# Kernel optimization log

Hardware: AMD Instinct MI355X
Metric: run time of the kernel (lower is better)

Reference implementation:

```python
import jax, jax.numpy as jnp
import numpy as np

B, P, Q, A, H = 8, 512, 64, 16, 128
H2, H10, G = 2 * H, 10 * H, 3 * H


def setup_inputs() -> dict:
    key = jax.random.key(0)
    ks = jax.random.split(key, 40)
    n = lambda k, s, sc=1.0: jax.random.normal(k, s, jnp.float32) * sc
    W = 0.05  # xavier-ish small init so tanh stays in linear-ish range
    inp = {
        "passage_enc": n(ks[0], (B, P, H2)),
        "query_enc": n(ks[1], (B, Q, H2)),
        "alt1_enc": n(ks[2], (B, A, H)),
        "alt2_enc": n(ks[3], (B, A, H)),
        "alt3_enc": n(ks[4], (B, A, H)),
        "a_att_w": n(ks[5], (H,), W),
        "Wc1": n(ks[6], (H2, H), W), "Wc2": n(ks[7], (H2, H), W), "vc": n(ks[8], (H,), W),
        "Wb": n(ks[9], (H2, H2), W),
        "Wd": n(ks[10], (H2, H), W), "vd": n(ks[11], (H,), W),
        "Wm": n(ks[12], (H2, H), W), "vm": n(ks[13], (H,), W),
        "wq": n(ks[14], (H2, H), W), "vq": n(ks[15], (H,), W),
        "wp1": n(ks[16], (H2, H), W), "wp2": n(ks[17], (H2, H), W), "vp": n(ks[18], (H,), W),
        "predict_w": n(ks[19], (H2, H), W),
        "gWih_f": n(ks[20], (H10, G), W), "gWhh_f": n(ks[21], (H, G), W),
        "gbih_f": jnp.zeros((G,), jnp.float32), "gbhh_f": jnp.zeros((G,), jnp.float32),
        "gWih_b": n(ks[22], (H10, G), W), "gWhh_b": n(ks[23], (H, G), W),
        "gbih_b": jnp.zeros((G,), jnp.float32), "gbhh_b": jnp.zeros((G,), jnp.float32),
        "passage_mask": jnp.ones((B, P), jnp.int32),
        "query_mask": jnp.ones((B, Q), jnp.int32),
        "alt1_mask": jnp.ones((B, A), jnp.int32),
        "alt2_mask": jnp.ones((B, A), jnp.int32),
        "alt3_mask": jnp.ones((B, A), jnp.int32),
    }
    return inp


def _att_pool(x, w, mask):
    # x: (B,T,D), w: (D,) -> (B,D) masked-softmax attention pooling
    s = jnp.where(mask != 0, x @ w, -jnp.inf)
    a = jax.nn.softmax(s, axis=1)
    return jnp.einsum('bt,btd->bd', a, x)


def _masked_attend(scores, qmask, query):
    # scores: (B,P,Q); mask over query axis, softmax over Q, weighted sum of query
    s = jnp.where(qmask[:, None, :] != 0, scores, -jnp.inf)
    a = jax.nn.softmax(s, axis=2)
    return jnp.einsum('bpq,bqd->bpd', a, query)


def _gru_dir(x, Wih, Whh, bih, bhh, reverse):
    # x: (B,T,Din) -> (B,T,H), PyTorch GRU gate convention
    if reverse:
        x = x[:, ::-1]
    gi = x @ Wih + bih  # (B,T,3H)
    h0 = jnp.zeros((x.shape[0], Whh.shape[0]), x.dtype)

    def step(h, gi_t):
        gh = h @ Whh + bhh
        i_r, i_z, i_n = jnp.split(gi_t, 3, axis=-1)
        h_r, h_z, h_n = jnp.split(gh, 3, axis=-1)
        r = jax.nn.sigmoid(i_r + h_r)
        z = jax.nn.sigmoid(i_z + h_z)
        nn_ = jnp.tanh(i_n + r * h_n)
        h_new = (1.0 - z) * nn_ + z * h
        return h_new, h_new

    _, ys = jax.lax.scan(step, h0, jnp.swapaxes(gi, 0, 1))
    ys = jnp.swapaxes(ys, 0, 1)
    if reverse:
        ys = ys[:, ::-1]
    return ys


def _forward(passage_enc, query_enc, alt1_enc, alt2_enc, alt3_enc,
             a_att_w, Wc1, Wc2, vc, Wb, Wd, vd, Wm, vm,
             wq, vq, wp1, wp2, vp, predict_w,
             gWih_f, gWhh_f, gbih_f, gbhh_f, gWih_b, gWhh_b, gbih_b, gbhh_b,
             passage_mask, query_mask, alt1_mask, alt2_mask, alt3_mask):
    # --- alternative-answer pooling ---
    a1 = _att_pool(alt1_enc, a_att_w, alt1_mask)
    a2 = _att_pool(alt2_enc, a_att_w, alt2_mask)
    a3 = _att_pool(alt3_enc, a_att_w, alt3_mask)

    # --- multi-hop passage-query attention (4 score variants) ---
    p1 = passage_enc @ Wc1          # (B,P,H)
    q1 = query_enc @ Wc2            # (B,Q,H)
    sc_c = jnp.einsum('bpqh,h->bpq', jnp.tanh(p1[:, :, None, :] + q1[:, None, :, :]), vc)
    pc = _masked_attend(sc_c, query_mask, query_enc)

    sc_b = jnp.einsum('bpd,bqd->bpq', passage_enc @ Wb, query_enc)
    pb = _masked_attend(sc_b, query_mask, query_enc)

    # Wd(p * q) with elementwise product, then tanh, then vd
    sc_d = jnp.einsum('bpqh,h->bpq',
                      jnp.tanh(jnp.einsum('bpk,bqk,kh->bpqh', passage_enc, query_enc, Wd)), vd)
    pd = _masked_attend(sc_d, query_mask, query_enc)

    # Wm(q - p) = q@Wm - p@Wm (linearity)
    pmq = query_enc @ Wm            # (B,Q,H)
    pmp = passage_enc @ Wm          # (B,P,H)
    sc_m = jnp.einsum('bpqh,h->bpq', jnp.tanh(pmq[:, None, :, :] - pmp[:, :, None, :]), vm)
    pm = _masked_attend(sc_m, query_mask, query_enc)

    # --- aggregation bi-GRU over (B,P,10H) ---
    agg_in = jnp.concatenate([passage_enc, pc, pb, pd, pm], axis=2)
    h_f = _gru_dir(agg_in, gWih_f, gWhh_f, gbih_f, gbhh_f, reverse=False)
    h_b = _gru_dir(agg_in, gWih_b, gWhh_b, gbih_b, gbhh_b, reverse=True)
    agg = jnp.concatenate([h_f, h_b], axis=2)   # (B,P,2H)

    # --- query summary rq ---
    sj = jnp.where(query_mask != 0, jnp.tanh(query_enc @ wq) @ vq, -jnp.inf)
    sj = jax.nn.softmax(sj, axis=1)
    rq = jnp.einsum('bq,bqd->bd', sj, query_enc)   # (B,2H)

    # --- passage summary rp attended by rq ---
    sp = jnp.tanh(agg @ wp1 + (rq @ wp2)[:, None, :]) @ vp   # (B,P)
    sp = jnp.where(passage_mask != 0, sp, -jnp.inf)
    sp = jax.nn.softmax(sp, axis=1)
    rp = jnp.einsum('bp,bpd->bd', sp, agg)          # (B,2H)
    rp = jax.nn.leaky_relu(rp @ predict_w)          # (B,H), slope 0.01

    alters = jnp.stack([a1, a2, a3], axis=1)        # (B,3,H)
    logits = jnp.einsum('bah,bh->ba', alters, rp)
    return jax.nn.softmax(logits, axis=1)


def reference(passage_enc, query_enc, alt1_enc, alt2_enc, alt3_enc,
              a_att_w, Wc1, Wc2, vc, Wb, Wd, vd, Wm, vm,
              wq, vq, wp1, wp2, vp, predict_w,
              gWih_f, gWhh_f, gbih_f, gbhh_f, gWih_b, gWhh_b, gbih_b, gbhh_b,
              passage_mask, query_mask, alt1_mask, alt2_mask, alt3_mask):
    return _forward(passage_enc, query_enc, alt1_enc, alt2_enc, alt3_enc,
                    a_att_w, Wc1, Wc2, vc, Wb, Wd, vd, Wm, vm,
                    wq, vq, wp1, wp2, vp, predict_w,
                    gWih_f, gWhh_f, gbih_f, gbhh_f, gWih_b, gWhh_b, gbih_b, gbhh_b,
                    passage_mask, query_mask, alt1_mask, alt2_mask, alt3_mask)
```

## Files before the change

kernel.cpp:

```cpp
#include <hip/hip_runtime.h>

#define B_ 8
#define P_ 512
#define Q_ 64
#define A_ 16
#define H_ 128
#define H2_ 256
#define H10_ 1280
#define G_ 384

typedef float f32x4 __attribute__((ext_vector_type(4)));
typedef _Float16 half4_t __attribute__((ext_vector_type(4)));
typedef _Float16 half8_t __attribute__((ext_vector_type(8)));

__device__ __forceinline__ float fast_tanh(float x) {
  return 1.f - 2.f * __builtin_amdgcn_rcpf(1.f + __builtin_amdgcn_exp2f(2.88539008f * x));
}
__device__ __forceinline__ float fast_sigm(float x) {
  return __builtin_amdgcn_rcpf(1.f + __builtin_amdgcn_exp2f(-1.44269504f * x));
}

#define GRUBAR() asm volatile("s_waitcnt lgkmcnt(0)\n\ts_barrier" ::: "memory")

#define NB_PRE 6936

__device__ __forceinline__ void prep_frag_body(int idx, const float* __restrict__ W,
                                               _Float16* __restrict__ out, int KT, int HT, int N) {
  int total = KT * HT * 64 * 4;
  if (idx >= total) return;
  int e = idx & 3;
  int l = (idx >> 2) & 63;
  int rest = idx >> 8;
  int ht = rest % HT;
  int ks = rest / HT;
  int k = ks * 16 + ((l >> 4) << 2) + e;
  int n = ht * 16 + (l & 15);
  out[idx] = (_Float16)W[(size_t)k * N + n];
}

__device__ __forceinline__ void prep_frag32_body(int idx, const float* __restrict__ W,
                                                 _Float16* __restrict__ out, int KT, int HT, int N) {
  int total = KT * HT * 64 * 8;
  if (idx >= total) return;
  int e = idx & 7;
  int l = (idx >> 3) & 63;
  int rest = idx >> 9;
  int ht = rest % HT;
  int ks = rest / HT;
  int k = ks * 32 + ((l >> 4) << 3) + e;
  int n = ht * 16 + (l & 15);
  out[idx] = (_Float16)W[(size_t)k * N + n];
}

__global__ __launch_bounds__(256) void k_pre(
    const float* __restrict__ a1, const float* __restrict__ a2, const float* __restrict__ a3,
    const int* __restrict__ m1, const int* __restrict__ m2, const int* __restrict__ m3,
    const float* __restrict__ a_att_w, float* __restrict__ alters,
    const float* __restrict__ Wd, _Float16* __restrict__ wd_sw,
    const float* __restrict__ gWih_f, const float* __restrict__ gWih_b,
    _Float16* __restrict__ gih_sw,
    const float* __restrict__ gWhh_f, const float* __restrict__ gWhh_b,
    _Float16* __restrict__ whh_sw,
    const float* __restrict__ pas, const float* __restrict__ qry,
    _Float16* __restrict__ pas_h,
    const float* __restrict__ Wc1, const float* __restrict__ Wm, const float* __restrict__ Wb,
    _Float16* __restrict__ wpc_sw,
    float* __restrict__ qryT,
    const float* __restrict__ Wc2, float* __restrict__ q1T, float* __restrict__ pmqT,
    const float* __restrict__ wq, const float* __restrict__ vq, float* __restrict__ sjraw) {
  int bx = blockIdx.x;
  int tid = threadIdx.x;
  if (bx < 24) {
    int b = bx / 3, i = bx % 3;
    const float* x = (i == 0) ? a1 : (i == 1) ? a2 : a3;
    const int* mk = (i == 0) ? m1 : (i == 1) ? m2 : m3;
    __shared__ float sc[A_];
    __shared__ float sw[A_];
    if (tid < A_) {
      const float* row = x + ((size_t)(b * A_ + tid)) * H_;
      float acc = 0.f;
      for (int h = 0; h < H_; ++h) acc += row[h] * a_att_w[h];
      sc[tid] = (mk[b * A_ + tid] != 0) ? acc : -1e30f;
    }
    __syncthreads();
    if (tid == 0) {
      float mx = -1e30f;
      for (int a = 0; a < A_; ++a) mx = fmaxf(mx, sc[a]);
      float s = 0.f;
      for (int a = 0; a < A_; ++a) { float e = __expf(sc[a] - mx); sw[a] = e; s += e; }
      float inv = 1.f / s;
      for (int a = 0; a < A_; ++a) sw[a] *= inv;
    }
    __syncthreads();
    if (tid < H_) {
      float acc = 0.f;
      for (int a = 0; a < A_; ++a) acc += sw[a] * x[((size_t)(b * A_ + a)) * H_ + tid];
      alters[((size_t)(b * 3 + i)) * H_ + tid] = acc;
    }
    return;
  }
  bx -= 24;
  if (bx < 128) { prep_frag_body(bx * 256 + tid, Wd, wd_sw, 16, 8, H_); return; }
  bx -= 128;
  if (bx < 1920) { prep_frag_body(bx * 256 + tid, gWih_f, gih_sw, 80, 24, G_); return; }
  bx -= 1920;
  if (bx < 1920) {
    prep_frag_body(bx * 256 + tid, gWih_b, gih_sw + (size_t)80 * 24 * 64 * 4, 80, 24, G_);
    return;
  }
  bx -= 1920;
  if (bx < 192) { prep_frag32_body(bx * 256 + tid, gWhh_f, whh_sw, 4, 24, G_); return; }
  bx -= 192;
  if (bx < 192) {
    prep_frag32_body(bx * 256 + tid, gWhh_b, whh_sw + (size_t)4 * 24 * 64 * 8, 4, 24, G_);
    return;
  }
  bx -= 192;
  if (bx < 1024) {
    int idx = bx * 256 + tid;
    float4 v = *(const float4*)(pas + (size_t)idx * 4);
    half4_t h;
    h[0] = (_Float16)v.x; h[1] = (_Float16)v.y; h[2] = (_Float16)v.z; h[3] = (_Float16)v.w;
    *(half4_t*)(pas_h + (size_t)idx * 4) = h;
    return;
  }
  bx -= 1024;
  if (bx < 512) {
    int idx = bx * 256 + tid;
    int e = idx & 3;
    int l = (idx >> 2) & 63;
    int rest = idx >> 8;
    int ht = rest & 31;
    int ks = rest >> 5;
    int k = ks * 16 + ((l >> 4) << 2) + e;
    int n = ht * 16 + (l & 15);
    float v = (n < 128) ? Wc1[(size_t)k * 128 + n]
            : (n < 256) ? Wm[(size_t)k * 128 + (n - 128)]
                        : Wb[(size_t)k * 256 + (n - 256)];
    wpc_sw[idx] = (_Float16)v;
    return;
  }
  bx -= 512;
  if (bx < 512) {
    int idx = bx * 256 + tid;
    int q = idx & 63;
    int d = (idx >> 6) & 255;
    int b = idx >> 14;
    qryT[idx] = qry[((size_t)(b * Q_ + q)) * H2_ + d];
    return;
  }
  bx -= 512;
  if (bx < 256) {
    int idx = bx * 256 + tid;
    int h = idx & 127;
    int rest = idx >> 7;
    int q = rest & 63;
    int b = rest >> 6;
    const float* qr = qry + ((size_t)(b * Q_ + q)) * H2_;
    float a1v = 0.f, a2v = 0.f;
#pragma unroll 4
    for (int d = 0; d < H2_; ++d) {
      float qv = qr[d];
      a1v += qv * Wc2[(size_t)d * H_ + h];
      a2v += qv * Wm[(size_t)d * H_ + h];
    }
    q1T[((size_t)(b * H_ + h)) * Q_ + q] = a1v;
    pmqT[((size_t)(b * H_ + h)) * Q_ + q] = a2v;
    return;
  }
  bx -= 256;
  {
    int rs = tid >> 7;
    int h = tid & 127;
    int row = bx * 2 + rs;
    const float* qr = qry + (size_t)row * H2_;
    float acc = 0.f;
#pragma unroll 4
    for (int d = 0; d < H2_; ++d) acc += qr[d] * wq[(size_t)d * H_ + h];
    float v = fast_tanh(acc) * vq[h];
    for (int m = 32; m >= 1; m >>= 1) v += __shfl_xor(v, m);
    __shared__ float par[2][2];
    if ((h & 63) == 0) par[rs][h >> 6] = v;
    __syncthreads();
    if (h == 0) sjraw[row] = par[rs][0] + par[rs][1];
  }
}

__global__ __launch_bounds__(256) void k_scd_rq(
    const float* __restrict__ pas, const float* __restrict__ qry,
    const _Float16* __restrict__ wd_sw, const float* __restrict__ vd,
    float* __restrict__ scd,
    const float* __restrict__ sjraw, const int* __restrict__ qmask,
    const float* __restrict__ wp2, float* __restrict__ rqw2,
    const _Float16* __restrict__ pas_h, const _Float16* __restrict__ wpc_sw,
    float* __restrict__ p1, float* __restrict__ pmp, float* __restrict__ pasWb) {
  int bx0 = blockIdx.x;
  int tid = threadIdx.x;
  if (bx0 < B_ * Q_ * 8) {
    int pt = bx0 & 7;
    int rem = bx0 >> 3;
    int q = rem & (Q_ - 1);
    int b = rem >> 6;
    int w = tid >> 6, l = tid & 63;
    __shared__ __align__(16) float qs[H2_];
    __shared__ float vds[H_];
    if (tid < H2_) qs[tid] = qry[((size_t)(b * Q_ + q)) * H2_ + tid];
    if (tid < H_) vds[tid] = vd[tid];
    __syncthreads();
    int arow = pt * 64 + w * 16 + (l & 15);
    const float* prow = pas + ((size_t)(b * P_) + arow) * H2_;
    int ko = (l >> 4) << 2;
    f32x4 acc[8] = {};
#pragma unroll
    for (int ks = 0; ks < 16; ++ks) {
      int j0 = ks * 16 + ko;
      float4 pa = *(const float4*)(prow + j0);
      float4 qa = *(const float4*)(qs + j0);
      half4_t a;
      a[0] = (_Float16)(pa.x * qa.x);
      a[1] = (_Float16)(pa.y * qa.y);
      a[2] = (_Float16)(pa.z * qa.z);
      a[3] = (_Float16)(pa.w * qa.w);
      const _Float16* bb = wd_sw + (((size_t)(ks * 8) * 64) + l) * 4;
#pragma unroll
      for (int ht = 0; ht < 8; ++ht) {
        half4_t bf = *(const half4_t*)(bb + (size_t)ht * 64 * 4);
        acc[ht] = __builtin_amdgcn_mfma_f32_16x16x16f16(a, bf, acc[ht], 0, 0, 0);
      }
    }
    float part[4] = {0.f, 0.f, 0.f, 0.f};
#pragma unroll
    for (int ht = 0; ht < 8; ++ht) {
      float v = vds[ht * 16 + (l & 15)];
#pragma unroll
      for (int j = 0; j < 4; ++j) part[j] += v * fast_tanh(acc[ht][j]);
    }
#pragma unroll
    for (int j = 0; j < 4; ++j) {
      float s = part[j];
      s += __shfl_xor(s, 1);
      s += __shfl_xor(s, 2);
      s += __shfl_xor(s, 4);
      s += __shfl_xor(s, 8);
      part[j] = s;
    }
    if ((l & 15) == 0) {
      int pr = pt * 64 + w * 16 + ((l >> 4) << 2);
#pragma unroll
      for (int j = 0; j < 4; ++j)
        scd[((size_t)b * P_ + pr + j) * Q_ + q] = part[j];
    }
    return;
  }
  if (bx0 < B_ * Q_ * 8 + B_) {
    int b = bx0 - B_ * Q_ * 8;
    int t = tid;
    __shared__ float sj[Q_];
    __shared__ float rql[H2_];
    if (t < Q_) {
      float s = (qmask[b * Q_ + t] != 0) ? sjraw[b * Q_ + t] : -1e30f;
      float mx = s;
      for (int m = 32; m >= 1; m >>= 1) mx = fmaxf(mx, __shfl_xor(mx, m));
      float e = __expf(s - mx);
      float sum = e;
      for (int m = 32; m >= 1; m >>= 1) sum += __shfl_xor(sum, m);
      sj[t] = e / sum;
    }
    __syncthreads();
    {
      float acc = 0.f;
      const float* qcol = qry + (size_t)b * Q_ * H2_ + t;
#pragma unroll 8
      for (int q = 0; q < Q_; ++q) acc += sj[q] * qcol[(size_t)q * H2_];
      rql[t] = acc;
    }
    __syncthreads();
    if (t < H_) {
      float acc = 0.f;
#pragma unroll 4
      for (int d = 0; d < H2_; ++d) acc += rql[d] * wp2[(size_t)d * H_ + t];
      rqw2[b * H_ + t] = acc;
    }
    return;
  }
  {
    int bx2 = bx0 - (B_ * Q_ * 8 + B_);
    int rt = bx2 >> 1, nh = bx2 & 1;
    int w = tid >> 6, l = tid & 63;
    int p0 = rt * 64 + w * 16;
    const _Float16* arow = pas_h + ((size_t)(p0 + (l & 15))) * H2_ + ((l >> 4) << 2);
    const _Float16* bbase = wpc_sw + (size_t)l * 4;
    f32x4 acc[16] = {};
    for (int ks = 0; ks < 16; ++ks) {
      half4_t a = *(const half4_t*)(arow + ks * 16);
      const _Float16* bkt = bbase + ((size_t)(ks * 32 + nh * 16)) * 64 * 4;
#pragma unroll
      for (int ht = 0; ht < 16; ++ht) {
        half4_t bf = *(const half4_t*)(bkt + (size_t)ht * 64 * 4);
        acc[ht] = __builtin_amdgcn_mfma_f32_16x16x16f16(a, bf, acc[ht], 0, 0, 0);
      }
    }
    int r0 = p0 + ((l >> 4) << 2);
#pragma unroll
    for (int ht = 0; ht < 16; ++ht) {
      int col = (nh * 16 + ht) * 16 + (l & 15);
#pragma unroll
      for (int j = 0; j < 4; ++j) {
        float v = acc[ht][j];
        size_t row = r0 + j;
        if (col < 128) p1[row * H_ + col] = v;
        else if (col < 256) pmp[row * H_ + (col - 128)] = v;
        else pasWb[row * H2_ + (col - 256)] = v;
      }
    }
  }
}

__global__ __launch_bounds__(256) void k_attend(
    const float* __restrict__ pas, const float* __restrict__ qry,
    const float* __restrict__ p1, const float* __restrict__ pmp,
    const float* __restrict__ q1T, const float* __restrict__ pmqT,
    const float* __restrict__ qryT,
    const float* __restrict__ pasWb, const float* __restrict__ scd,
    const float* __restrict__ vc, const float* __restrict__ vm,
    const int* __restrict__ qmask, _Float16* __restrict__ agg_h) {
  int bx = blockIdx.x;
  int b = bx >> 9, p = bx & (P_ - 1);
  int tid = threadIdx.x;
  __shared__ float p1s[H_], pmps[H_];
  __shared__ float pbs[H2_];
  __shared__ float sscd[Q_];
  __shared__ float ps[3][4][Q_];
  __shared__ float asw[4][Q_];
  size_t rowp = (size_t)b * P_ + p;
  if (tid < H_) {
    p1s[tid] = p1[rowp * H_ + tid];
    pmps[tid] = pmp[rowp * H_ + tid];
  }
  if (tid < H2_) pbs[tid] = pasWb[rowp * H2_ + tid];
  if (tid < Q_) sscd[tid] = scd[rowp * Q_ + tid];
  __syncthreads();
  {
    int q = tid & 63, part = tid >> 6;
    const float* q1b = q1T + (size_t)b * H_ * Q_;
    const float* pmqb = pmqT + (size_t)b * H_ * Q_;
    const float* qTb = qryT + (size_t)b * H2_ * Q_;
    float s_c = 0.f, s_m = 0.f, s_b = 0.f;
    int h0 = part * 32;
#pragma unroll 4
    for (int i = 0; i < 32; ++i) {
      int h = h0 + i;
      s_c += fast_tanh(p1s[h] + q1b[h * Q_ + q]) * vc[h];
      s_m += fast_tanh(pmqb[h * Q_ + q] - pmps[h]) * vm[h];
    }
    int d0 = part * 64;
#pragma unroll 4
    for (int i = 0; i < 64; ++i) {
      int d = d0 + i;
      s_b += pbs[d] * qTb[d * Q_ + q];
    }
    ps[0][part][q] = s_c;
    ps[1][part][q] = s_b;
    ps[2][part][q] = s_m;
  }
  __syncthreads();
  {
    int wv = tid >> 6, lane = tid & 63;
    float s;
    if (wv == 2) s = sscd[lane];
    else {
      int arr = (wv == 3) ? 2 : wv;
      s = (ps[arr][0][lane] + ps[arr][1][lane]) + (ps[arr][2][lane] + ps[arr][3][lane]);
    }
    s = (qmask[b * Q_ + lane] != 0) ? s : -1e30f;
    float mx = s;
    for (int m = 32; m >= 1; m >>= 1) mx = fmaxf(mx, __shfl_xor(mx, m));
    float e = __expf(s - mx);
    float sum = e;
    for (int m = 32; m >= 1; m >>= 1) sum += __shfl_xor(sum, m);
    asw[wv][lane] = e / sum;
  }
  __syncthreads();
  {
    int d = tid;
    const float* qcol = qry + (size_t)b * Q_ * H2_ + d;
    float o0 = 0.f, o1 = 0.f, o2 = 0.f, o3 = 0.f;
#pragma unroll 8
    for (int q2 = 0; q2 < Q_; ++q2) {
      float qv = qcol[(size_t)q2 * H2_];
      o0 += asw[0][q2] * qv;
      o1 += asw[1][q2] * qv;
      o2 += asw[2][q2] * qv;
      o3 += asw[3][q2] * qv;
    }
    _Float16* arow = agg_h + rowp * H10_;
    arow[d] = (_Float16)pas[rowp * H2_ + d];
    arow[256 + d] = (_Float16)o0;
    arow[512 + d] = (_Float16)o1;
    arow[768 + d] = (_Float16)o2;
    arow[1024 + d] = (_Float16)o3;
  }
}

__global__ __launch_bounds__(256) void k_gi(
    const _Float16* __restrict__ agg_h, const _Float16* __restrict__ gih_sw,
    const float* __restrict__ gbih_f, const float* __restrict__ gbih_b,
    float* __restrict__ gi_f, float* __restrict__ gi_b) {
  int dir = blockIdx.y;
  const float* gbih = dir ? gbih_b : gbih_f;
  float* gi = dir ? gi_b : gi_f;
  int tid = threadIdx.x;
  int w = tid >> 6, l = tid & 63;
  int p0 = blockIdx.x * 64 + w * 16;
  const _Float16* arow = agg_h + ((size_t)(p0 + (l & 15))) * H10_ + ((l >> 4) << 2);
  const _Float16* bbase = gih_sw + (size_t)dir * 80 * 24 * 64 * 4 + (size_t)l * 4;
  f32x4 acc[24] = {};
  for (int ks = 0; ks < 80; ++ks) {
    half4_t a = *(const half4_t*)(arow + ks * 16);
    const _Float16* bkt = bbase + (size_t)ks * 24 * 64 * 4;
#pragma unroll
    for (int ht = 0; ht < 24; ++ht) {
      half4_t bf = *(const half4_t*)(bkt + (size_t)ht * 64 * 4);
      acc[ht] = __builtin_amdgcn_mfma_f32_16x16x16f16(a, bf, acc[ht], 0, 0, 0);
    }
  }
  int r0 = p0 + ((l >> 4) << 2);
#pragma unroll
  for (int ht = 0; ht < 24; ++ht) {
    int col = ht * 16 + (l & 15);
    float bias = gbih[col];
#pragma unroll
    for (int j = 0; j < 4; ++j)
      gi[((size_t)(r0 + j)) * G_ + col] = acc[ht][j] + bias;
  }
}

__global__ __attribute__((amdgpu_waves_per_eu(2, 2))) __launch_bounds__(512) void k_gru(
    const float* __restrict__ gi_f, const float* __restrict__ gi_b,
    const _Float16* __restrict__ whh_sw,
    const float* __restrict__ bhh_f, const float* __restrict__ bhh_b,
    float* __restrict__ agg) {
  int dir = blockIdx.x >> 3;
  int bb = blockIdx.x & 7;
  const float* gi = dir ? gi_b : gi_f;
  const float* bhh = dir ? bhh_b : bhh_f;
  int tid = threadIdx.x;
  int w = tid >> 6, l = tid & 63;
  int j = w * 16 + (l & 15);
  half8_t Bf[3][4];
  {
    const _Float16* wb = whh_sw + (size_t)dir * 4 * 24 * 64 * 8;
#pragma unroll
    for (int g = 0; g < 3; ++g) {
      int ct = g * 8 + w;
#pragma unroll
      for (int ks = 0; ks < 4; ++ks)
        Bf[g][ks] = *(const half8_t*)(wb + (((size_t)(ks * 24 + ct)) * 64 + l) * 8);
    }
  }
  float bhr = bhh[j], bhz = bhh[128 + j], bhn = bhh[256 + j];
  __shared__ __align__(16) _Float16 hsbuf[2][H_];
  if (tid < H_) hsbuf[0][tid] = (_Float16)0.f;
  float hprev = 0.f;
  int p = dir ? (P_ - 1) : 0;
  int dp = dir ? -1 : 1;
  size_t gbase = (size_t)bb * P_;
  float g0r, g0z, g0n, g1r, g1z, g1n;
  {
    size_t r0 = (gbase + p) * G_;
    g0r = gi[r0 + j]; g0z = gi[r0 + 128 + j]; g0n = gi[r0 + 256 + j];
    size_t r1 = (gbase + p + dp) * G_;
    g1r = gi[r1 + j]; g1z = gi[r1 + 128 + j]; g1n = gi[r1 + 256 + j];
  }
  GRUBAR();
  int cur = 0;
  int ao = (l >> 4) << 3;
  for (int t = 0; t < P_; ++t) {
    float g2r = 0.f, g2z = 0.f, g2n = 0.f;
    if (t + 2 < P_) {
      size_t r2 = (gbase + p + 2 * dp) * G_;
      g2r = gi[r2 + j]; g2z = gi[r2 + 128 + j]; g2n = gi[r2 + 256 + j];
    }
    const _Float16* hb = hsbuf[cur];
    half8_t ha[4];
#pragma unroll
    for (int ks = 0; ks < 4; ++ks) ha[ks] = *(const half8_t*)(hb + ks * 32 + ao);
    f32x4 arL = {}, arH = {}, azL = {}, azH = {}, anL = {}, anH = {};
    arL = __builtin_amdgcn_mfma_f32_16x16x32_f16(ha[0], Bf[0][0], arL, 0, 0, 0);
    azL = __builtin_amdgcn_mfma_f32_16x16x32_f16(ha[0], Bf[1][0], azL, 0, 0, 0);
    anL = __builtin_amdgcn_mfma_f32_16x16x32_f16(ha[0], Bf[2][0], anL, 0, 0, 0);
    arH = __builtin_amdgcn_mfma_f32_16x16x32_f16(ha[2], Bf[0][2], arH, 0, 0, 0);
    azH = __builtin_amdgcn_mfma_f32_16x16x32_f16(ha[2], Bf[1][2], azH, 0, 0, 0);
    anH = __builtin_amdgcn_mfma_f32_16x16x32_f16(ha[2], Bf[2][2], anH, 0, 0, 0);
    arL = __builtin_amdgcn_mfma_f32_16x16x32_f16(ha[1], Bf[0][1], arL, 0, 0, 0);
    azL = __builtin_amdgcn_mfma_f32_16x16x32_f16(ha[1], Bf[1][1], azL, 0, 0, 0);
    anL = __builtin_amdgcn_mfma_f32_16x16x32_f16(ha[1], Bf[2][1], anL, 0, 0, 0);
    arH = __builtin_amdgcn_mfma_f32_16x16x32_f16(ha[3], Bf[0][3], arH, 0, 0, 0);
    azH = __builtin_amdgcn_mfma_f32_16x16x32_f16(ha[3], Bf[1][3], azH, 0, 0, 0);
    anH = __builtin_amdgcn_mfma_f32_16x16x32_f16(ha[3], Bf[2][3], anH, 0, 0, 0);
    float arS = arL[0] + arH[0];
    float azS = azL[0] + azH[0];
    float anS = anL[0] + anH[0];
    float r = fast_sigm(g0r + arS + bhr);
    float z = fast_sigm(g0z + azS + bhz);
    float nn = fast_tanh(g0n + r * (anS + bhn));
    float hnew = (1.f - z) * nn + z * hprev;
    hprev = hnew;
    if (l < 16) {
      hsbuf[cur ^ 1][j] = (_Float16)hnew;
      agg[(size_t)(gbase + p) * H2_ + dir * H_ + j] = hnew;
    }
    GRUBAR();
    cur ^= 1;
    g0r = g1r; g0z = g1z; g0n = g1n;
    g1r = g2r; g1z = g2z; g1n = g2n;
    p += dp;
  }
}

__global__ __launch_bounds__(128) void k_spscore(
    const float* __restrict__ agg, const float* __restrict__ wp1,
    const float* __restrict__ rqw2, const float* __restrict__ vp,
    float* __restrict__ spraw) {
  int bx = blockIdx.x;
  int b = bx >> 9, p = bx & (P_ - 1);
  int h = threadIdx.x;
  const float* ar = agg + ((size_t)b * P_ + p) * H2_;
  float acc = rqw2[b * H_ + h];
#pragma unroll 8
  for (int d = 0; d < H2_; ++d) acc += ar[d] * wp1[(size_t)d * H_ + h];
  float v = fast_tanh(acc) * vp[h];
  for (int m = 32; m >= 1; m >>= 1) v += __shfl_xor(v, m);
  __shared__ float par[2];
  if ((h & 63) == 0) par[h >> 6] = v;
  __syncthreads();
  if (h == 0) spraw[bx] = par[0] + par[1];
}

__global__ __launch_bounds__(256) void k_final(
    const float* __restrict__ spraw, const int* __restrict__ pmask,
    const float* __restrict__ agg, const float* __restrict__ predict_w,
    const float* __restrict__ alters, float* __restrict__ out) {
  int b = blockIdx.x;
  int t = threadIdx.x;
  __shared__ float sp[P_];
  __shared__ float red[4];
  __shared__ float rpr[H2_];
  __shared__ float rpl[H_];
  __shared__ float lg[3];
  float s0 = (pmask[b * P_ + t] != 0) ? spraw[b * P_ + t] : -1e30f;
  float s1 = (pmask[b * P_ + 256 + t] != 0) ? spraw[b * P_ + 256 + t] : -1e30f;
  float mx = fmaxf(s0, s1);
  for (int m = 32; m >= 1; m >>= 1) mx = fmaxf(mx, __shfl_xor(mx, m));
  if ((t & 63) == 0) red[t >> 6] = mx;
  __syncthreads();
  mx = fmaxf(fmaxf(red[0], red[1]), fmaxf(red[2], red[3]));
  float e0 = __expf(s0 - mx), e1 = __expf(s1 - mx);
  float ss = e0 + e1;
  for (int m = 32; m >= 1; m >>= 1) ss += __shfl_xor(ss, m);
  __syncthreads();
  if ((t & 63) == 0) red[t >> 6] = ss;
  __syncthreads();
  float tot = red[0] + red[1] + red[2] + red[3];
  float inv = 1.f / tot;
  sp[t] = e0 * inv;
  sp[256 + t] = e1 * inv;
  __syncthreads();
  {
    float acc = 0.f;
    const float* acol = agg + (size_t)b * P_ * H2_ + t;
#pragma unroll 8
    for (int p = 0; p < P_; ++p) acc += sp[p] * acol[(size_t)p * H2_];
    rpr[t] = acc;
  }
  __syncthreads();
  if (t < H_) {
    float acc = 0.f;
#pragma unroll 4
    for (int d = 0; d < H2_; ++d) acc += rpr[d] * predict_w[(size_t)d * H_ + t];
    rpl[t] = (acc > 0.f) ? acc : 0.01f * acc;
  }
  __syncthreads();
  if (t < 3) {
    float acc = 0.f;
    const float* al = alters + ((size_t)(b * 3 + t)) * H_;
    for (int h = 0; h < H_; ++h) acc += al[h] * rpl[h];
    lg[t] = acc;
  }
  __syncthreads();
  if (t == 0) {
    float m3 = fmaxf(lg[0], fmaxf(lg[1], lg[2]));
    float x0 = __expf(lg[0] - m3), x1 = __expf(lg[1] - m3), x2 = __expf(lg[2] - m3);
    float is = 1.f / (x0 + x1 + x2);
    out[b * 3 + 0] = x0 * is;
    out[b * 3 + 1] = x1 * is;
    out[b * 3 + 2] = x2 * is;
  }
}

extern "C" void kernel_launch(void* const* d_in, const int* in_sizes, int n_in,
                              void* d_out, int out_size, void* d_ws, size_t ws_size,
                              hipStream_t stream) {
  (void)in_sizes; (void)n_in; (void)out_size; (void)ws_size;
  const float* pas = (const float*)d_in[0];
  const float* qry = (const float*)d_in[1];
  const float* alt1 = (const float*)d_in[2];
  const float* alt2 = (const float*)d_in[3];
  const float* alt3 = (const float*)d_in[4];
  const float* a_att_w = (const float*)d_in[5];
  const float* Wc1 = (const float*)d_in[6];
  const float* Wc2 = (const float*)d_in[7];
  const float* vc = (const float*)d_in[8];
  const float* Wb = (const float*)d_in[9];
  const float* Wd = (const float*)d_in[10];
  const float* vd = (const float*)d_in[11];
  const float* Wm = (const float*)d_in[12];
  const float* vm = (const float*)d_in[13];
  const float* wq = (const float*)d_in[14];
  const float* vq = (const float*)d_in[15];
  const float* wp1 = (const float*)d_in[16];
  const float* wp2 = (const float*)d_in[17];
  const float* vp = (const float*)d_in[18];
  const float* predict_w = (const float*)d_in[19];
  const float* gWih_f = (const float*)d_in[20];
  const float* gWhh_f = (const float*)d_in[21];
  const float* gbih_f = (const float*)d_in[22];
  const float* gbhh_f = (const float*)d_in[23];
  const float* gWih_b = (const float*)d_in[24];
  const float* gWhh_b = (const float*)d_in[25];
  const float* gbih_b = (const float*)d_in[26];
  const float* gbhh_b = (const float*)d_in[27];
  const int* pmask = (const int*)d_in[28];
  const int* qmask = (const int*)d_in[29];
  const int* m1 = (const int*)d_in[30];
  const int* m2 = (const int*)d_in[31];
  const int* m3 = (const int*)d_in[32];
  float* out = (float*)d_out;

  char* ws = (char*)d_ws;
  size_t off = 0;
  auto alloc_f = [&](size_t n) {
    float* ptr = (float*)(ws + off);
    off += n * 4;
    off = (off + 255) & ~(size_t)255;
    return ptr;
  };
  float* alters = alloc_f((size_t)B_ * 3 * H_);
  float* p1 = alloc_f((size_t)B_ * P_ * H_);
  float* pmp = alloc_f((size_t)B_ * P_ * H_);
  float* pasWb = alloc_f((size_t)B_ * P_ * H2_);
  float* scd = alloc_f((size_t)B_ * P_ * Q_);
  float* gi_f = alloc_f((size_t)B_ * P_ * G_);
  float* gi_b = alloc_f((size_t)B_ * P_ * G_);
  float* agg = alloc_f((size_t)B_ * P_ * H2_);
  float* sjraw = alloc_f((size_t)B_ * Q_);
  float* rqw2 = alloc_f((size_t)B_ * H_);
  float* spraw = alloc_f((size_t)B_ * P_);
  float* q1T = alloc_f((size_t)B_ * H_ * Q_);
  float* pmqT = alloc_f((size_t)B_ * H_ * Q_);
  float* qryT = alloc_f((size_t)B_ * H2_ * Q_);
  auto alloc_h = [&](size_t n) {
    _Float16* ptr = (_Float16*)(ws + off);
    off += n * 2;
    off = (off + 255) & ~(size_t)255;
    return ptr;
  };
  _Float16* wd_sw = alloc_h((size_t)16 * 8 * 64 * 4);
  _Float16* gih_sw = alloc_h((size_t)2 * 80 * 24 * 64 * 4);
  _Float16* agg_h = alloc_h((size_t)B_ * P_ * H10_);
  _Float16* whh_sw = alloc_h((size_t)2 * 4 * 24 * 64 * 8);
  _Float16* pas_h = alloc_h((size_t)B_ * P_ * H2_);
  _Float16* wpc_sw = alloc_h((size_t)16 * 32 * 64 * 4);

  k_pre<<<NB_PRE, 256, 0, stream>>>(
      alt1, alt2, alt3, m1, m2, m3, a_att_w, alters,
      Wd, wd_sw, gWih_f, gWih_b, gih_sw, gWhh_f, gWhh_b, whh_sw,
      pas, qry, pas_h, Wc1, Wm, Wb, wpc_sw, qryT, Wc2, q1T, pmqT, wq, vq, sjraw);
  k_scd_rq<<<B_ * Q_ * 8 + B_ + 128, 256, 0, stream>>>(
      pas, qry, wd_sw, vd, scd, sjraw, qmask, wp2, rqw2,
      pas_h, wpc_sw, p1, pmp, pasWb);
  k_attend<<<B_ * P_, 256, 0, stream>>>(
      pas, qry, p1, pmp, q1T, pmqT, qryT, pasWb, scd, vc, vm, qmask, agg_h);
  k_gi<<<dim3(64, 2), 256, 0, stream>>>(agg_h, gih_sw, gbih_f, gbih_b, gi_f, gi_b);
  k_gru<<<16, 512, 0, stream>>>(gi_f, gi_b, whh_sw, gbhh_f, gbhh_b, agg);
  k_spscore<<<B_ * P_, 128, 0, stream>>>(agg, wp1, rqw2, vp, spraw);
  k_final<<<B_, 256, 0, stream>>>(spraw, pmask, agg, predict_w, alters, out);
}
```

Baseline: 608.8 us.

## Process multiple rows per block in attend/spscore and halve GRU waves

k_attend now handles two passage rows per block, so each loaded query-side column (q1T, pmqT, qryT, qry) serves two rows. k_spscore handles eight rows per block, reusing each wp1 load across eight accumulators. The GRU recurrence drops from 8 to 4 waves per block, each wave computing two 16-column tiles, which shrinks the per-step barrier but doubles the serial MFMA chain per wave. This adds register pressure and reduces grid parallelism in the attend and spscore kernels.

After: 661.5 us. 1.09x slower.

```diff
diff --git a/kernel.cpp b/kernel.cpp
--- a/kernel.cpp
+++ b/kernel.cpp
@@ -325,80 +325,111 @@
     const float* __restrict__ vc, const float* __restrict__ vm,
     const int* __restrict__ qmask, _Float16* __restrict__ agg_h) {
   int bx = blockIdx.x;
-  int b = bx >> 9, p = bx & (P_ - 1);
+  int b = bx >> 8, p0 = (bx & 255) * 2;
   int tid = threadIdx.x;
-  __shared__ float p1s[H_], pmps[H_];
-  __shared__ float pbs[H2_];
-  __shared__ float sscd[Q_];
-  __shared__ float ps[3][4][Q_];
-  __shared__ float asw[4][Q_];
-  size_t rowp = (size_t)b * P_ + p;
-  if (tid < H_) {
-    p1s[tid] = p1[rowp * H_ + tid];
-    pmps[tid] = pmp[rowp * H_ + tid];
-  }
-  if (tid < H2_) pbs[tid] = pasWb[rowp * H2_ + tid];
-  if (tid < Q_) sscd[tid] = scd[rowp * Q_ + tid];
+  __shared__ float p1s[2][H_], pmps[2][H_];
+  __shared__ float pbs[2][H2_];
+  __shared__ float sscd[2][Q_];
+  __shared__ float ps[2][3][4][Q_];
+  __shared__ float asw[2][4][Q_];
+  size_t rowp = (size_t)b * P_ + p0;
+  if (tid < 2 * H_) {
+    int pp = tid >> 7, h = tid & 127;
+    p1s[pp][h] = p1[(rowp + pp) * H_ + h];
+    pmps[pp][h] = pmp[(rowp + pp) * H_ + h];
+  }
+  {
+    int pp = tid >> 7, d2 = (tid & 127) * 2;
+    pbs[pp][d2] = pasWb[(rowp + pp) * H2_ + d2];
+    pbs[pp][d2 + 1] = pasWb[(rowp + pp) * H2_ + d2 + 1];
+  }
+  if (tid < 2 * Q_) sscd[tid >> 6][tid & 63] = scd[(rowp + (tid >> 6)) * Q_ + (tid & 63)];
   __syncthreads();
   {
     int q = tid & 63, part = tid >> 6;
     const float* q1b = q1T + (size_t)b * H_ * Q_;
     const float* pmqb = pmqT + (size_t)b * H_ * Q_;
     const float* qTb = qryT + (size_t)b * H2_ * Q_;
-    float s_c = 0.f, s_m = 0.f, s_b = 0.f;
+    float sc0 = 0.f, sc1 = 0.f, sm0 = 0.f, sm1 = 0.f, sb0 = 0.f, sb1 = 0.f;
     int h0 = part * 32;
 #pragma unroll 4
     for (int i = 0; i < 32; ++i) {
       int h = h0 + i;
-      s_c += fast_tanh(p1s[h] + q1b[h * Q_ + q]) * vc[h];
-      s_m += fast_tanh(pmqb[h * Q_ + q] - pmps[h]) * vm[h];
+      float q1v = q1b[h * Q_ + q];
+      float pmqv = pmqb[h * Q_ + q];
+      float vcv = vc[h], vmv = vm[h];
+      sc0 += fast_tanh(p1s[0][h] + q1v) * vcv;
+      sc1 += fast_tanh(p1s[1][h] + q1v) * vcv;
+      sm0 += fast_tanh(pmqv - pmps[0][h]) * vmv;
+      sm1 += fast_tanh(pmqv - pmps[1][h]) * vmv;
     }
     int d0 = part * 64;
 #pragma unroll 4
     for (int i = 0; i < 64; ++i) {
       int d = d0 + i;
-      s_b += pbs[d] * qTb[d * Q_ + q];
-    }
-    ps[0][part][q] = s_c;
-    ps[1][part][q] = s_b;
-    ps[2][part][q] = s_m;
+      float qv = qTb[d * Q_ + q];
+      sb0 += pbs[0][d] * qv;
+      sb1 += pbs[1][d] * qv;
+    }
+    ps[0][0][part][q] = sc0;
+    ps[1][0][part][q] = sc1;
+    ps[0][1][part][q] = sb0;
+    ps[1][1][part][q] = sb1;
+    ps[0][2][part][q] = sm0;
+    ps[1][2][part][q] = sm1;
   }
   __syncthreads();
   {
     int wv = tid >> 6, lane = tid & 63;
-    float s;
-    if (wv == 2) s = sscd[lane];
-    else {
-      int arr = (wv == 3) ? 2 : wv;
-      s = (ps[arr][0][lane] + ps[arr][1][lane]) + (ps[arr][2][lane] + ps[arr][3][lane]);
-    }
-    s = (qmask[b * Q_ + lane] != 0) ? s : -1e30f;
-    float mx = s;
-    for (int m = 32; m >= 1; m >>= 1) mx = fmaxf(mx, __shfl_xor(mx, m));
-    float e = __expf(s - mx);
-    float sum = e;
-    for (int m = 32; m >= 1; m >>= 1) sum += __shfl_xor(sum, m);
-    asw[wv][lane] = e / sum;
+    int msk = (qmask[b * Q_ + lane] != 0);
+#pragma unroll
+    for (int pp = 0; pp < 2; ++pp) {
+      float s;
+      if (wv == 2) s = sscd[pp][lane];
+      else {
+        int arr = (wv == 3) ? 2 : wv;
+        s = (ps[pp][arr][0][lane] + ps[pp][arr][1][lane]) +
+            (ps[pp][arr][2][lane] + ps[pp][arr][3][lane]);
+      }
+      s = msk ? s : -1e30f;
+      float mx = s;
+      for (int m = 32; m >= 1; m >>= 1) mx = fmaxf(mx, __shfl_xor(mx, m));
+      float e = __expf(s - mx);
+      float sum = e;
+      for (int m = 32; m >= 1; m >>= 1) sum += __shfl_xor(sum, m);
+      asw[pp][wv][lane] = e / sum;
+    }
   }
   __syncthreads();
   {
     int d = tid;
     const float* qcol = qry + (size_t)b * Q_ * H2_ + d;
-    float o0 = 0.f, o1 = 0.f, o2 = 0.f, o3 = 0.f;
+    float o00 = 0.f, o01 = 0.f, o02 = 0.f, o03 = 0.f;
+    float o10 = 0.f, o11 = 0.f, o12 = 0.f, o13 = 0.f;
 #pragma unroll 8
     for (int q2 = 0; q2 < Q_; ++q2) {
       float qv = qcol[(size_t)q2 * H2_];
-      o0 += asw[0][q2] * qv;
-      o1 += asw[1][q2] * qv;
-      o2 += asw[2][q2] * qv;
-      o3 += asw[3][q2] * qv;
-    }
-    _Float16* arow = agg_h + rowp * H10_;
-    arow[d] = (_Float16)pas[rowp * H2_ + d];
-    arow[256 + d] = (_Float16)o0;
-    arow[512 + d] = (_Float16)o1;
-    arow[768 + d] = (_Float16)o2;
-    arow[1024 + d] = (_Float16)o3;
+      o00 += asw[0][0][q2] * qv;
+      o01 += asw[0][1][q2] * qv;
+      o02 += asw[0][2][q2] * qv;
+      o03 += asw[0][3][q2] * qv;
+      o10 += asw[1][0][q2] * qv;
+      o11 += asw[1][1][q2] * qv;
+      o12 += asw[1][2][q2] * qv;
+      o13 += asw[1][3][q2] * qv;
+    }
+    _Float16* arow0 = agg_h + rowp * H10_;
+    arow0[d] = (_Float16)pas[rowp * H2_ + d];
+    arow0[256 + d] = (_Float16)o00;
+    arow0[512 + d] = (_Float16)o01;
+    arow0[768 + d] = (_Float16)o02;
+    arow0[1024 + d] = (_Float16)o03;
+    _Float16* arow1 = agg_h + (rowp + 1) * H10_;
+    arow1[d] = (_Float16)pas[(rowp + 1) * H2_ + d];
+    arow1[256 + d] = (_Float16)o10;
+    arow1[512 + d] = (_Float16)o11;
+    arow1[768 + d] = (_Float16)o12;
+    arow1[1024 + d] = (_Float16)o13;
   }
 }
 
@@ -435,7 +466,7 @@
   }
 }
 
-__global__ __attribute__((amdgpu_waves_per_eu(2, 2))) __launch_bounds__(512) void k_gru(
+__global__ __attribute__((amdgpu_waves_per_eu(1, 1))) __launch_bounds__(256) void k_gru(
     const float* __restrict__ gi_f, const float* __restrict__ gi_b,
     const _Float16* __restrict__ whh_sw,
     const float* __restrict__ bhh_f, const float* __restrict__ bhh_b,
@@ -446,74 +477,83 @@
   const float* bhh = dir ? bhh_b : bhh_f;
   int tid = threadIdx.x;
   int w = tid >> 6, l = tid & 63;
-  int j = w * 16 + (l & 15);
-  half8_t Bf[3][4];
+  int j0 = w * 32 + (l & 15);
+  int j1 = j0 + 16;
+  half8_t Bf[3][2][4];
   {
     const _Float16* wb = whh_sw + (size_t)dir * 4 * 24 * 64 * 8;
 #pragma unroll
-    for (int g = 0; g < 3; ++g) {
-      int ct = g * 8 + w;
-#pragma unroll
-      for (int ks = 0; ks < 4; ++ks)
-        Bf[g][ks] = *(const half8_t*)(wb + (((size_t)(ks * 24 + ct)) * 64 + l) * 8);
-    }
-  }
-  float bhr = bhh[j], bhz = bhh[128 + j], bhn = bhh[256 + j];
+    for (int g = 0; g < 3; ++g)
+#pragma unroll
+      for (int cc = 0; cc < 2; ++cc) {
+        int ct = g * 8 + w * 2 + cc;
+#pragma unroll
+        for (int ks = 0; ks < 4; ++ks)
+          Bf[g][cc][ks] = *(const half8_t*)(wb + (((size_t)(ks * 24 + ct)) * 64 + l) * 8);
+      }
+  }
+  float bhr0 = bhh[j0], bhz0 = bhh[128 + j0], bhn0 = bhh[256 + j0];
+  float bhr1 = bhh[j1], bhz1 = bhh[128 + j1], bhn1 = bhh[256 + j1];
   __shared__ __align__(16) _Float16 hsbuf[2][H_];
   if (tid < H_) hsbuf[0][tid] = (_Float16)0.f;
-  float hprev = 0.f;
+  float hprev0 = 0.f, hprev1 = 0.f;
   int p = dir ? (P_ - 1) : 0;
   int dp = dir ? -1 : 1;
   size_t gbase = (size_t)bb * P_;
-  float g0r, g0z, g0n, g1r, g1z, g1n;
+  float g0[6], g1[6];
   {
     size_t r0 = (gbase + p) * G_;
-    g0r = gi[r0 + j]; g0z = gi[r0 + 128 + j]; g0n = gi[r0 + 256 + j];
+    g0[0] = gi[r0 + j0]; g0[1] = gi[r0 + 128 + j0]; g0[2] = gi[r0 + 256 + j0];
+    g0[3] = gi[r0 + j1]; g0[4] = gi[r0 + 128 + j1]; g0[5] = gi[r0 + 256 + j1];
     size_t r1 = (gbase + p + dp) * G_;
-    g1r = gi[r1 + j]; g1z = gi[r1 + 128 + j]; g1n = gi[r1 + 256 + j];
+    g1[0] = gi[r1 + j0]; g1[1] = gi[r1 + 128 + j0]; g1[2] = gi[r1 + 256 + j0];
+    g1[3] = gi[r1 + j1]; g1[4] = gi[r1 + 128 + j1]; g1[5] = gi[r1 + 256 + j1];
   }
   GRUBAR();
   int cur = 0;
   int ao = (l >> 4) << 3;
   for (int t = 0; t < P_; ++t) {
-    float g2r = 0.f, g2z = 0.f, g2n = 0.f;
+    float g2[6] = {};
     if (t + 2 < P_) {
       size_t r2 = (gbase + p + 2 * dp) * G_;
-      g2r = gi[r2 + j]; g2z = gi[r2 + 128 + j]; g2n = gi[r2 + 256 + j];
+      g2[0] = gi[r2 + j0]; g2[1] = gi[r2 + 128 + j0]; g2[2] = gi[r2 + 256 + j0];
+      g2[3] = gi[r2 + j1]; g2[4] = gi[r2 + 128 + j1]; g2[5] = gi[r2 + 256 + j1];
     }
     const _Float16* hb = hsbuf[cur];
     half8_t ha[4];
 #pragma unroll
     for (int ks = 0; ks < 4; ++ks) ha[ks] = *(const half8_t*)(hb + ks * 32 + ao);
-    f32x4 arL = {}, arH = {}, azL = {}, azH = {}, anL = {}, anH = {};
-    arL = __builtin_amdgcn_mfma_f32_16x16x32_f16(ha[0], Bf[0][0], arL, 0, 0, 0);
-    azL = __builtin_amdgcn_mfma_f32_16x16x32_f16(ha[0], Bf[1][0], azL, 0, 0, 0);
-    anL = __builtin_amdgcn_mfma_f32_16x16x32_f16(ha[0], Bf[2][0], anL, 0, 0, 0);
-    arH = __builtin_amdgcn_mfma_f32_16x16x32_f16(ha[2], Bf[0][2], arH, 0, 0, 0);
-    azH = __builtin_amdgcn_mfma_f32_16x16x32_f16(ha[2], Bf[1][2], azH, 0, 0, 0);
-    anH = __builtin_amdgcn_mfma_f32_16x16x32_f16(ha[2], Bf[2][2], anH, 0, 0, 0);
-    arL = __builtin_amdgcn_mfma_f32_16x16x32_f16(ha[1], Bf[0][1], arL, 0, 0, 0);
-    azL = __builtin_amdgcn_mfma_f32_16x16x32_f16(ha[1], Bf[1][1], azL, 0, 0, 0);
-    anL = __builtin_amdgcn_mfma_f32_16x16x32_f16(ha[1], Bf[2][1], anL, 0, 0, 0);
-    arH = __builtin_amdgcn_mfma_f32_16x16x32_f16(ha[3], Bf[0][3], arH, 0, 0, 0);
-    azH = __builtin_amdgcn_mfma_f32_16x16x32_f16(ha[3], Bf[1][3], azH, 0, 0, 0);
-    anH = __builtin_amdgcn_mfma_f32_16x16x32_f16(ha[3], Bf[2][3], anH, 0, 0, 0);
-    float arS = arL[0] + arH[0];
-    float azS = azL[0] + azH[0];
-    float anS = anL[0] + anH[0];
-    float r = fast_sigm(g0r + arS + bhr);
-    float z = fast_sigm(g0z + azS + bhz);
-    float nn = fast_tanh(g0n + r * (anS + bhn));
-    float hnew = (1.f - z) * nn + z * hprev;
-    hprev = hnew;
+    f32x4 ar0 = {}, ar1 = {}, az0 = {}, az1 = {}, an0 = {}, an1 = {};
+#pragma unroll
+    for (int ks = 0; ks < 4; ++ks) {
+      ar0 = __builtin_amdgcn_mfma_f32_16x16x32_f16(ha[ks], Bf[0][0][ks], ar0, 0, 0, 0);
+      az0 = __builtin_amdgcn_mfma_f32_16x16x32_f16(ha[ks], Bf[1][0][ks], az0, 0, 0, 0);
+      an0 = __builtin_amdgcn_mfma_f32_16x16x32_f16(ha[ks], Bf[2][0][ks], an0, 0, 0, 0);
+      ar1 = __builtin_amdgcn_mfma_f32_16x16x32_f16(ha[ks], Bf[0][1][ks], ar1, 0, 0, 0);
+      az1 = __builtin_amdgcn_mfma_f32_16x16x32_f16(ha[ks], Bf[1][1][ks], az1, 0, 0, 0);
+      an1 = __builtin_amdgcn_mfma_f32_16x16x32_f16(ha[ks], Bf[2][1][ks], an1, 0, 0, 0);
+    }
+    float r0v = fast_sigm(g0[0] + ar0[0] + bhr0);
+    float z0v = fast_sigm(g0[1] + az0[0] + bhz0);
+    float n0v = fast_tanh(g0[2] + r0v * (an0[0] + bhn0));
+    float h0v = (1.f - z0v) * n0v + z0v * hprev0;
+    float r1v = fast_sigm(g0[3] + ar1[0] + bhr1);
+    float z1v = fast_sigm(g0[4] + az1[0] + bhz1);
+    float n1v = fast_tanh(g0[5] + r1v * (an1[0] + bhn1));
+    float h1v = (1.f - z1v) * n1v + z1v * hprev1;
+    hprev0 = h0v;
+    hprev1 = h1v;
     if (l < 16) {
-      hsbuf[cur ^ 1][j] = (_Float16)hnew;
-      agg[(size_t)(gbase + p) * H2_ + dir * H_ + j] = hnew;
+      hsbuf[cur ^ 1][j0] = (_Float16)h0v;
+      hsbuf[cur ^ 1][j1] = (_Float16)h1v;
+      float* arow = agg + (size_t)(gbase + p) * H2_ + dir * H_;
+      arow[j0] = h0v;
+      arow[j1] = h1v;
     }
     GRUBAR();
     cur ^= 1;
-    g0r = g1r; g0z = g1z; g0n = g1n;
-    g1r = g2r; g1z = g2z; g1n = g2n;
+#pragma unroll
+    for (int i = 0; i < 6; ++i) { g0[i] = g1[i]; g1[i] = g2[i]; }
     p += dp;
   }
 }
@@ -523,18 +563,29 @@
     const float* __restrict__ rqw2, const float* __restrict__ vp,
     float* __restrict__ spraw) {
   int bx = blockIdx.x;
-  int b = bx >> 9, p = bx & (P_ - 1);
+  int b = bx >> 6, p0 = (bx & 63) * 8;
   int h = threadIdx.x;
-  const float* ar = agg + ((size_t)b * P_ + p) * H2_;
-  float acc = rqw2[b * H_ + h];
-#pragma unroll 8
-  for (int d = 0; d < H2_; ++d) acc += ar[d] * wp1[(size_t)d * H_ + h];
-  float v = fast_tanh(acc) * vp[h];
-  for (int m = 32; m >= 1; m >>= 1) v += __shfl_xor(v, m);
-  __shared__ float par[2];
-  if ((h & 63) == 0) par[h >> 6] = v;
-  __syncthreads();
-  if (h == 0) spraw[bx] = par[0] + par[1];
+  const float* ar = agg + ((size_t)b * P_ + p0) * H2_;
+  float base = rqw2[b * H_ + h];
+  float acc[8];
+#pragma unroll
+  for (int r = 0; r < 8; ++r) acc[r] = base;
+#pragma unroll 4
+  for (int d = 0; d < H2_; ++d) {
+    float wv = wp1[(size_t)d * H_ + h];
+#pragma unroll
+    for (int r = 0; r < 8; ++r) acc[r] += ar[(size_t)r * H2_ + d] * wv;
+  }
+  __shared__ float par[8][2];
+  float vph = vp[h];
+#pragma unroll
+  for (int r = 0; r < 8; ++r) {
+    float v = fast_tanh(acc[r]) * vph;
+    for (int m = 32; m >= 1; m >>= 1) v += __shfl_xor(v, m);
+    if ((h & 63) == 0) par[r][h >> 6] = v;
+  }
+  __syncthreads();
+  if (h < 8) spraw[(size_t)b * P_ + p0 + h] = par[h][0] + par[h][1];
 }
 
 __global__ __launch_bounds__(256) void k_final(
@@ -679,10 +730,10 @@
   k_scd_rq<<<B_ * Q_ * 8 + B_ + 128, 256, 0, stream>>>(
       pas, qry, wd_sw, vd, scd, sjraw, qmask, wp2, rqw2,
       pas_h, wpc_sw, p1, pmp, pasWb);
-  k_attend<<<B_ * P_, 256, 0, stream>>>(
+  k_attend<<<B_ * P_ / 2, 256, 0, stream>>>(
       pas, qry, p1, pmp, q1T, pmqT, qryT, pasWb, scd, vc, vm, qmask, agg_h);
   k_gi<<<dim3(64, 2), 256, 0, stream>>>(agg_h, gih_sw, gbih_f, gbih_b, gi_f, gi_b);
-  k_gru<<<16, 512, 0, stream>>>(gi_f, gi_b, whh_sw, gbhh_f, gbhh_b, agg);
-  k_spscore<<<B_ * P_, 128, 0, stream>>>(agg, wp1, rqw2, vp, spraw);
+  k_gru<<<16, 256, 0, stream>>>(gi_f, gi_b, whh_sw, gbhh_f, gbhh_b, agg);
+  k_spscore<<<B_ * P_ / 8, 128, 0, stream>>>(agg, wp1, rqw2, vp, spraw);
   k_final<<<B_, 256, 0, stream>>>(spraw, pmask, agg, predict_w, alters, out);
 }
```
